# Optimization experiments

Measured on AMD Instinct MI355X. Metric: run time of the kernel, lower is better.

Reference implementation:

```python
import jax, jax.numpy as jnp
import numpy as np

B, S, D_IN, D_VQ, V = 8, 2048, 768, 256, 8192
TEMP = 1.0  # registered buffer, relu(1.0) = 1.0


def setup_inputs() -> dict:
    key = jax.random.key(0)
    k1, k2, k3 = jax.random.split(key, 3)
    x = jax.random.normal(k1, (B, S, D_IN), dtype=jnp.float32)
    W = jax.random.normal(k2, (D_VQ, D_IN), dtype=jnp.float32) * 0.02  # linear weight
    b = jnp.zeros((D_VQ,), dtype=jnp.float32)
    table = jax.random.normal(k3, (V, D_VQ), dtype=jnp.float32)  # learnable_table ~ randn
    return {"x": x, "W": W, "b": b, "table": table}


def reference(x, W, b, table):
    # x: [B,S,D_IN] -> h: [B,S,D_VQ]
    h = jnp.einsum('bsi,di->bsd', x, W) + b
    # negative squared L2 distance to each code: -(|h|^2 + |c|^2 - 2 h.c)
    sim = -(jnp.sum(h * h, axis=-1, keepdims=True)
            + jnp.sum(table * table, axis=-1)
            - 2.0 * jnp.einsum('bsd,vd->bsv', h, table))  # [B,S,V]
    sim = jax.nn.relu(jnp.float32(TEMP)) * sim
    p_code = jax.nn.softmax(sim, axis=-1)
    picked_idx = jnp.argmax(p_code, axis=-1)  # [B,S]
    onehot = jax.nn.one_hot(picked_idx, V, dtype=p_code.dtype)
    # straight-through: hard one-hot forward, soft softmax backward
    p_hard = p_code + jax.lax.stop_gradient(onehot - p_code)
    picked_code = jnp.einsum('bsv,vd->bsd', p_hard, table)  # F.linear(p_hard, table.T)
    # vq_code = x + picked_code - x.detach()  (== picked_code in value)
    vq_code = h + picked_code - jax.lax.stop_gradient(h)
    return vq_code
```

## Files before the change

### kernel.cpp

```cpp
#include <hip/hip_runtime.h>


typedef float f32x4 __attribute__((ext_vector_type(4)));
typedef short s16x8 __attribute__((ext_vector_type(8)));
typedef short s16x4 __attribute__((ext_vector_type(4)));

#define M_TOTAL 16384
#define KDIM 768
#define DQ 256
#define NV 8192
#define MARGIN 1.5f
#define CPB 2048u

#define OFF_TBF   0u
#define OFF_WH    4194304u
#define OFF_WL    4587520u
#define OFF_C2    4980736u
#define OFF_M     5013504u
#define OFF_BEST  5079040u
#define OFF_BCNT  5210112u
#define OFF_CAND  5214208u
#define WS_SINGLE (OFF_CAND + 1024u * CPB * 8u)

static __device__ inline unsigned short bf_rne(float f) {
  unsigned u = __float_as_uint(f);
  u += 0x7FFFu + ((u >> 16) & 1u);
  return (unsigned short)(u >> 16);
}
static __device__ inline unsigned short bf_tr(float f) {
  return (unsigned short)(__float_as_uint(f) >> 16);
}
static __device__ inline float bf_up(unsigned short s) {
  return __uint_as_float(((unsigned)s) << 16);
}
static __device__ inline unsigned mono(float f) {
  unsigned u = __float_as_uint(f);
  return (u & 0x80000000u) ? ~u : (u | 0x80000000u);
}
static __device__ inline float demono(unsigned k) {
  unsigned u = (k & 0x80000000u) ? (k ^ 0x80000000u) : ~k;
  return __uint_as_float(u);
}
static __device__ inline f32x4 mfma16(s16x8 a, s16x8 b, f32x4 c) {
  return __builtin_amdgcn_mfma_f32_16x16x32_bf16(a, b, c, 0, 0, 0);
}

#define PB_TBF 1024
#define PB_C2  32
#define PB_W   192
#define PB_INIT 64

__global__ __launch_bounds__(256) void prep_kernel(
    const float* __restrict__ Wm, const float* __restrict__ table,
    unsigned char* __restrict__ ws) {
  unsigned short* tbf = (unsigned short*)(ws + OFF_TBF);
  unsigned short* Wh  = (unsigned short*)(ws + OFF_WH);
  unsigned short* Wl  = (unsigned short*)(ws + OFF_WL);
  float* c2 = (float*)(ws + OFF_C2);
  unsigned* Mu = (unsigned*)(ws + OFF_M);
  unsigned long long* best = (unsigned long long*)(ws + OFF_BEST);
  const int b = blockIdx.x, t = threadIdx.x;
  if (b < PB_TBF) {
    size_t e0 = ((size_t)b * 256 + t) * 8;
    float4 f0 = *(const float4*)(table + e0);
    float4 f1 = *(const float4*)(table + e0 + 4);
    s16x8 v;
    v[0]=(short)bf_rne(f0.x); v[1]=(short)bf_rne(f0.y);
    v[2]=(short)bf_rne(f0.z); v[3]=(short)bf_rne(f0.w);
    v[4]=(short)bf_rne(f1.x); v[5]=(short)bf_rne(f1.y);
    v[6]=(short)bf_rne(f1.z); v[7]=(short)bf_rne(f1.w);
    *(s16x8*)(tbf + e0) = v;
  } else if (b < PB_TBF + PB_C2) {
    const int v = (b - PB_TBF) * 256 + t;
    const float4* row = (const float4*)(table + (size_t)v * DQ);
    float s = 0.f;
    for (int q = 0; q < 64; ++q) {
      float4 x = row[q];
      s = fmaf(x.x, x.x, s); s = fmaf(x.y, x.y, s);
      s = fmaf(x.z, x.z, s); s = fmaf(x.w, x.w, s);
    }
    c2[v] = s;
  } else if (b < PB_TBF + PB_C2 + PB_W) {
    size_t i = ((size_t)(b - PB_TBF - PB_C2) * 256 + t) * 4;
    float4 f = *(const float4*)(Wm + i);
    float fv[4] = {f.x, f.y, f.z, f.w};
    s16x4 vh, vl;
#pragma unroll
    for (int q = 0; q < 4; ++q) {
      unsigned short hi = bf_tr(fv[q]);
      vh[q] = (short)hi;
      vl[q] = (short)bf_rne(fv[q] - bf_up(hi));
    }
    *(s16x4*)(Wh + i) = vh;
    *(s16x4*)(Wl + i) = vl;
  } else {
    const int i = (b - PB_TBF - PB_C2 - PB_W) * 256 + t;
    Mu[i] = 0u;
    best[i] = 0ull;
  }
}

__global__ __launch_bounds__(256, 3) void h_gemm_kernel(
    const float* __restrict__ x, const float* __restrict__ bias,
    const unsigned char* __restrict__ ws, float* __restrict__ hout) {
  const unsigned short* Whp = (const unsigned short*)(ws + OFF_WH);
  const unsigned short* Wlp = (const unsigned short*)(ws + OFF_WL);
  __shared__ unsigned short xh[128 * 40], xl[128 * 40];
  __shared__ unsigned short wh[64 * 40],  wl[64 * 40];
  const int t = threadIdx.x;
  const int lane = t & 63, wid = t >> 6;
  const int g = lane >> 4, lm = lane & 15;
  const int row_tile = blockIdx.x >> 2, col_tile = blockIdx.x & 3;
  const int r_ld = t >> 1, half = t & 1;
  const int n_ld = t >> 2, qtr = t & 3;

  f32x4 acc[2][4];
#pragma unroll
  for (int i = 0; i < 2; ++i)
#pragma unroll
    for (int j = 0; j < 4; ++j) acc[i][j] = (f32x4)0.f;

  const float* xsrc = x + (size_t)(row_tile * 128 + r_ld) * KDIM + half * 16;
  const unsigned short* whs = Whp + (size_t)(col_tile * 64 + n_ld) * KDIM + qtr * 8;
  const unsigned short* wls = Wlp + (size_t)(col_tile * 64 + n_ld) * KDIM + qtr * 8;

  float4 px[4]; s16x8 pwh, pwl;
#pragma unroll
  for (int q = 0; q < 4; ++q) px[q] = *(const float4*)(xsrc + q * 4);
  pwh = *(const s16x8*)(whs);
  pwl = *(const s16x8*)(wls);

  for (int kc = 0; kc < KDIM / 32; ++kc) {
    __syncthreads();
    {
      float fv[16] = {px[0].x, px[0].y, px[0].z, px[0].w,
                      px[1].x, px[1].y, px[1].z, px[1].w,
                      px[2].x, px[2].y, px[2].z, px[2].w,
                      px[3].x, px[3].y, px[3].z, px[3].w};
      s16x8 vh0, vh1, vl0, vl1;
#pragma unroll
      for (int e = 0; e < 8; ++e) {
        unsigned short hi = bf_tr(fv[e]);
        vh0[e] = (short)hi; vl0[e] = (short)bf_rne(fv[e] - bf_up(hi));
      }
#pragma unroll
      for (int e = 0; e < 8; ++e) {
        unsigned short hi = bf_tr(fv[8 + e]);
        vh1[e] = (short)hi; vl1[e] = (short)bf_rne(fv[8 + e] - bf_up(hi));
      }
      const int xb = r_ld * 40 + half * 16;
      *(s16x8*)&xh[xb] = vh0; *(s16x8*)&xh[xb + 8] = vh1;
      *(s16x8*)&xl[xb] = vl0; *(s16x8*)&xl[xb + 8] = vl1;
      const int wb = n_ld * 40 + qtr * 8;
      *(s16x8*)&wh[wb] = pwh;
      *(s16x8*)&wl[wb] = pwl;
    }
    if (kc + 1 < KDIM / 32) {
      const int k0 = (kc + 1) * 32;
#pragma unroll
      for (int q = 0; q < 4; ++q) px[q] = *(const float4*)(xsrc + k0 + q * 4);
      pwh = *(const s16x8*)(whs + k0);
      pwl = *(const s16x8*)(wls + k0);
    }
    __syncthreads();
    s16x8 ah[2], al[2], bh[4], bl[4];
#pragma unroll
    for (int fr = 0; fr < 2; ++fr) {
      const int rb2 = (wid * 32 + fr * 16 + lm) * 40 + g * 8;
      ah[fr] = *(const s16x8*)&xh[rb2];
      al[fr] = *(const s16x8*)&xl[rb2];
    }
#pragma unroll
    for (int fc = 0; fc < 4; ++fc) {
      const int cb = (fc * 16 + lm) * 40 + g * 8;
      bh[fc] = *(const s16x8*)&wh[cb];
      bl[fc] = *(const s16x8*)&wl[cb];
    }
#pragma unroll
    for (int fr = 0; fr < 2; ++fr)
#pragma unroll
      for (int fc = 0; fc < 4; ++fc) {
        acc[fr][fc] = mfma16(ah[fr], bh[fc], acc[fr][fc]);
        acc[fr][fc] = mfma16(ah[fr], bl[fc], acc[fr][fc]);
        acc[fr][fc] = mfma16(al[fr], bh[fc], acc[fr][fc]);
      }
  }
#pragma unroll
  for (int fc = 0; fc < 4; ++fc) {
    const int col_g = col_tile * 64 + fc * 16 + lm;
    const float bv = bias[col_g];
#pragma unroll
    for (int fr = 0; fr < 2; ++fr) {
      const int row_base = row_tile * 128 + wid * 32 + fr * 16 + g * 4;
#pragma unroll
      for (int r = 0; r < 4; ++r)
        hout[(size_t)(row_base + r) * DQ + col_g] = acc[fr][fc][r] + bv;
    }
  }
}

__global__ __launch_bounds__(256, 3) void scan6_kernel(
    const float* __restrict__ h, const float* __restrict__ table,
    unsigned char* __restrict__ ws) {
  const unsigned short* tbf = (const unsigned short*)(ws + OFF_TBF);
  const float* c2 = (const float*)(ws + OFF_C2);
  unsigned* Mu = (unsigned*)(ws + OFF_M);
  unsigned long long* best = (unsigned long long*)(ws + OFF_BEST);
  unsigned* bcnt = (unsigned*)(ws + OFF_BCNT);
  uint2* cand = (uint2*)(ws + OFF_CAND) + (size_t)blockIdx.x * CPB;
  __shared__ unsigned short bt[2][32 * 256];
  __shared__ unsigned lcnt;

  const int t = threadIdx.x, lane = t & 63, wid = t >> 6;
  const int g4 = lane >> 4, lm = lane & 15;
  const int rb = blockIdx.x >> 3, sp = blockIdx.x & 7;
  const int wrow = rb * 128 + wid * 32;
  const int code0 = sp * 1024;

  if (t == 0) lcnt = 0u;

  s16x8 ah[2][8];
#pragma unroll
  for (int fr = 0; fr < 2; ++fr) {
    const float* hp = h + (size_t)(wrow + fr * 16 + lm) * DQ + g4 * 8;
#pragma unroll
    for (int ks = 0; ks < 8; ++ks) {
      float4 a0 = *(const float4*)(hp + ks * 32);
      float4 a1 = *(const float4*)(hp + ks * 32 + 4);
      s16x8 v;
      v[0]=(short)bf_tr(a0.x); v[1]=(short)bf_tr(a0.y);
      v[2]=(short)bf_tr(a0.z); v[3]=(short)bf_tr(a0.w);
      v[4]=(short)bf_tr(a1.x); v[5]=(short)bf_tr(a1.y);
      v[6]=(short)bf_tr(a1.z); v[7]=(short)bf_tr(a1.w);
      ah[fr][ks] = v;
    }
  }

  float rm[2][4];
#pragma unroll
  for (int fr = 0; fr < 2; ++fr)
#pragma unroll
    for (int r = 0; r < 4; ++r) rm[fr][r] = -3.4e38f;

  int psrc[4], pdst[4];
#pragma unroll
  for (int p = 0; p < 4; ++p) {
    const int o = p * 4096 + t * 16;
    const int code = o >> 9, gsw = (o >> 4) & 31;
    const int gsrc = gsw ^ (code & 7);
    psrc[p] = code * 256 + gsrc * 8;
    pdst[p] = p * 2048 + t * 8;
  }
  const unsigned short* sbase = tbf + (size_t)code0 * DQ;

#define STAGE(buf, tilev)                                                     \
  {                                                                           \
    const unsigned short* s0 = sbase + (size_t)(tilev) * 8192;                \
    _Pragma("unroll")                                                         \
    for (int p = 0; p < 4; ++p)                                               \
      __builtin_amdgcn_global_load_lds(                                       \
          (const unsigned int*)(s0 + psrc[p]),                                \
          (unsigned int*)&bt[buf][pdst[p]], 16, 0, 0);                        \
  }

  STAGE(0, 0);
  __syncthreads();
  int cur = 0;

  for (int tile = 0; tile < 32; ++tile) {
    if (tile + 1 < 32) STAGE(cur ^ 1, tile + 1);

    f32x4 acc[2][2];
#pragma unroll
    for (int fr = 0; fr < 2; ++fr)
#pragma unroll
      for (int fc = 0; fc < 2; ++fc) acc[fr][fc] = (f32x4)0.f;

#pragma unroll
    for (int ks = 0; ks < 8; ++ks) {
      const int gb = ks * 4 + g4;
      const int c0 = lm,      gr0 = gb ^ (c0 & 7);
      const int c1 = 16 + lm, gr1 = gb ^ (c1 & 7);
      s16x8 b0 = *(const s16x8*)&bt[cur][c0 * 256 + gr0 * 8];
      s16x8 b1 = *(const s16x8*)&bt[cur][c1 * 256 + gr1 * 8];
      acc[0][0] = mfma16(ah[0][ks], b0, acc[0][0]);
      acc[1][0] = mfma16(ah[1][ks], b0, acc[1][0]);
      acc[0][1] = mfma16(ah[0][ks], b1, acc[0][1]);
      acc[1][1] = mfma16(ah[1][ks], b1, acc[1][1]);
    }

    float sc[2][2][4];
#pragma unroll
    for (int fc = 0; fc < 2; ++fc) {
      const float cc = c2[code0 + tile * 32 + fc * 16 + lm];
#pragma unroll
      for (int fr = 0; fr < 2; ++fr)
#pragma unroll
        for (int r = 0; r < 4; ++r) {
          const float s = fmaf(2.f, acc[fr][fc][r], -cc);
          sc[fr][fc][r] = s;
          rm[fr][r] = fmaxf(rm[fr][r], s);
        }
    }
#pragma unroll
    for (int fr = 0; fr < 2; ++fr)
#pragma unroll
      for (int r = 0; r < 4; ++r) {
        float v = rm[fr][r];
        v = fmaxf(v, __shfl_xor(v, 1));
        v = fmaxf(v, __shfl_xor(v, 2));
        v = fmaxf(v, __shfl_xor(v, 4));
        v = fmaxf(v, __shfl_xor(v, 8));
        rm[fr][r] = v;
      }

#pragma unroll
    for (int fc = 0; fc < 2; ++fc) {
      const unsigned code_g = (unsigned)(code0 + tile * 32 + fc * 16 + lm);
#pragma unroll
      for (int fr = 0; fr < 2; ++fr)
#pragma unroll
        for (int r = 0; r < 4; ++r) {
          if (sc[fr][fc][r] >= rm[fr][r] - MARGIN) {
            const unsigned row_g = (unsigned)(wrow + fr * 16 + g4 * 4 + r);
            const unsigned idx = atomicAdd(&lcnt, 1u);
            if (idx < CPB) {
              uint2 e;
              e.x = (row_g << 13) | code_g;
              e.y = __float_as_uint(sc[fr][fc][r]);
              cand[idx] = e;
            } else {
              const float4* hp4 = (const float4*)(h + (size_t)row_g * DQ);
              const float4* tp4 = (const float4*)(table + (size_t)code_g * DQ);
              float dot = 0.f;
#pragma unroll 4
              for (int q = 0; q < 64; ++q) {
                float4 a = hp4[q], bb = tp4[q];
                dot = fmaf(a.x, bb.x, dot); dot = fmaf(a.y, bb.y, dot);
                dot = fmaf(a.z, bb.z, dot); dot = fmaf(a.w, bb.w, dot);
              }
              const float sx = fmaf(2.f, dot, -c2[code_g]);
              const unsigned long long key =
                  ((unsigned long long)mono(sx) << 32) |
                  (unsigned long long)(0xFFFFFFFFu - code_g);
              atomicMax(&best[row_g], key);
            }
          }
        }
    }

    __syncthreads();
    cur ^= 1;
  }
#undef STAGE

#pragma unroll
  for (int fr = 0; fr < 2; ++fr)
#pragma unroll
    for (int r = 0; r < 4; ++r)
      if (lm == 0) atomicMax(&Mu[wrow + fr * 16 + g4 * 4 + r], mono(rm[fr][r]));

  __syncthreads();
  if (t == 0) bcnt[blockIdx.x] = (lcnt < CPB) ? lcnt : CPB;
}

__global__ __launch_bounds__(256) void rescore_kernel(
    const float* __restrict__ h, const float* __restrict__ table,
    unsigned char* __restrict__ ws) {
  const float* c2 = (const float*)(ws + OFF_C2);
  const unsigned* Mu = (const unsigned*)(ws + OFF_M);
  unsigned long long* best = (unsigned long long*)(ws + OFF_BEST);
  const unsigned* bcnt = (const unsigned*)(ws + OFF_BCNT);
  const uint2* cand = (const uint2*)(ws + OFF_CAND) + (size_t)blockIdx.x * CPB;

  const unsigned count = bcnt[blockIdx.x];
  const int g = threadIdx.x & 15;
  const unsigned grp = threadIdx.x >> 4;

  for (unsigned i = grp; i < count; i += 16) {
    const uint2 e = cand[i];
    const unsigned row = e.x >> 13, code = e.x & 8191u;
    const float sbf = __uint_as_float(e.y);
    if (sbf < demono(Mu[row]) - MARGIN) continue;
    const float4* hp = (const float4*)(h + (size_t)row * DQ);
    const float4* tp = (const float4*)(table + (size_t)code * DQ);
    float dot = 0.f;
#pragma unroll
    for (int q = 0; q < 4; ++q) {
      float4 a = hp[g * 4 + q], b = tp[g * 4 + q];
      dot = fmaf(a.x, b.x, dot); dot = fmaf(a.y, b.y, dot);
      dot = fmaf(a.z, b.z, dot); dot = fmaf(a.w, b.w, dot);
    }
    dot += __shfl_xor(dot, 1);
    dot += __shfl_xor(dot, 2);
    dot += __shfl_xor(dot, 4);
    dot += __shfl_xor(dot, 8);
    if (g == 0) {
      const float sx = fmaf(2.f, dot, -c2[code]);
      const unsigned long long key =
          ((unsigned long long)mono(sx) << 32) |
          (unsigned long long)(0xFFFFFFFFu - code);
      atomicMax(&best[row], key);
    }
  }
}

template<int MODE>
__global__ __launch_bounds__(256, 3) void scan3_kernel(
    const float* __restrict__ h, const float* __restrict__ table,
    unsigned char* __restrict__ ws) {
  const unsigned short* tbf = (const unsigned short*)(ws + OFF_TBF);
  const float* c2 = (const float*)(ws + OFF_C2);
  unsigned* Mu = (unsigned*)(ws + OFF_M);
  unsigned long long* best = (unsigned long long*)(ws + OFF_BEST);
  __shared__ unsigned short bt[2][32 * 256];

  const int t = threadIdx.x, lane = t & 63, wid = t >> 6;
  const int g4 = lane >> 4, lm = lane & 15;
  const int rb = blockIdx.x >> 3, sp = blockIdx.x & 7;
  const int wrow = rb * 128 + wid * 32;
  const int code0 = sp * 1024;

  s16x8 ah[2][8];
#pragma unroll
  for (int fr = 0; fr < 2; ++fr) {
    const float* hp = h + (size_t)(wrow + fr * 16 + lm) * DQ + g4 * 8;
#pragma unroll
    for (int ks = 0; ks < 8; ++ks) {
      float4 a0 = *(const float4*)(hp + ks * 32);
      float4 a1 = *(const float4*)(hp + ks * 32 + 4);
      s16x8 v;
      v[0]=(short)bf_tr(a0.x); v[1]=(short)bf_tr(a0.y);
      v[2]=(short)bf_tr(a0.z); v[3]=(short)bf_tr(a0.w);
      v[4]=(short)bf_tr(a1.x); v[5]=(short)bf_tr(a1.y);
      v[6]=(short)bf_tr(a1.z); v[7]=(short)bf_tr(a1.w);
      ah[fr][ks] = v;
    }
  }

  float rm[2][4];
#pragma unroll
  for (int fr = 0; fr < 2; ++fr)
#pragma unroll
    for (int r = 0; r < 4; ++r) {
      if (MODE == 2) rm[fr][r] = -3.4e38f;
      else           rm[fr][r] = demono(Mu[wrow + fr * 16 + g4 * 4 + r]);
    }

  int psrc[4], pdst[4];
#pragma unroll
  for (int p = 0; p < 4; ++p) {
    const int o = p * 4096 + t * 16;
    const int code = o >> 9, gsw = (o >> 4) & 31;
    const int gsrc = gsw ^ (code & 7);
    psrc[p] = code * 256 + gsrc * 8;
    pdst[p] = p * 2048 + t * 8;
  }
  const unsigned short* sbase = tbf + (size_t)code0 * DQ;

#define STAGE(buf, tilev)                                                     \
  {                                                                           \
    const unsigned short* s0 = sbase + (size_t)(tilev) * 8192;                \
    _Pragma("unroll")                                                         \
    for (int p = 0; p < 4; ++p)                                               \
      __builtin_amdgcn_global_load_lds(                                       \
          (const unsigned int*)(s0 + psrc[p]),                                \
          (unsigned int*)&bt[buf][pdst[p]], 16, 0, 0);                        \
  }

  STAGE(0, 0);
  __syncthreads();
  int cur = 0;

  for (int tile = 0; tile < 32; ++tile) {
    if (tile + 1 < 32) STAGE(cur ^ 1, tile + 1);

    f32x4 acc[2][2];
#pragma unroll
    for (int fr = 0; fr < 2; ++fr)
#pragma unroll
      for (int fc = 0; fc < 2; ++fc) acc[fr][fc] = (f32x4)0.f;

#pragma unroll
    for (int ks = 0; ks < 8; ++ks) {
      const int gb = ks * 4 + g4;
      const int c0 = lm,      gr0 = gb ^ (c0 & 7);
      const int c1 = 16 + lm, gr1 = gb ^ (c1 & 7);
      s16x8 b0 = *(const s16x8*)&bt[cur][c0 * 256 + gr0 * 8];
      s16x8 b1 = *(const s16x8*)&bt[cur][c1 * 256 + gr1 * 8];
      acc[0][0] = mfma16(ah[0][ks], b0, acc[0][0]);
      acc[1][0] = mfma16(ah[1][ks], b0, acc[1][0]);
      acc[0][1] = mfma16(ah[0][ks], b1, acc[0][1]);
      acc[1][1] = mfma16(ah[1][ks], b1, acc[1][1]);
    }

#pragma unroll
    for (int fc = 0; fc < 2; ++fc) {
      const int code_g = code0 + tile * 32 + fc * 16 + lm;
      const float cc = c2[code_g];
#pragma unroll
      for (int fr = 0; fr < 2; ++fr)
#pragma unroll
        for (int r = 0; r < 4; ++r) {
          const float s = fmaf(2.f, acc[fr][fc][r], -cc);
          if (MODE == 2) {
            rm[fr][r] = fmaxf(rm[fr][r], s);
          } else {
            if (s >= rm[fr][r] - MARGIN) {
              const int row_g = wrow + fr * 16 + g4 * 4 + r;
              const float4* hp4 = (const float4*)(h + (size_t)row_g * DQ);
              const float4* tp4 = (const float4*)(table + (size_t)code_g * DQ);
              float dot = 0.f;
#pragma unroll 4
              for (int q = 0; q < 64; ++q) {
                float4 a = hp4[q], bb = tp4[q];
                dot = fmaf(a.x, bb.x, dot); dot = fmaf(a.y, bb.y, dot);
                dot = fmaf(a.z, bb.z, dot); dot = fmaf(a.w, bb.w, dot);
              }
              const float sx = fmaf(2.f, dot, -cc);
              const unsigned long long key =
                  ((unsigned long long)mono(sx) << 32) |
                  (unsigned long long)(0xFFFFFFFFu - (unsigned)code_g);
              atomicMax(&best[row_g], key);
            }
          }
        }
    }

    __syncthreads();
    cur ^= 1;
  }
#undef STAGE

  if (MODE == 2) {
#pragma unroll
    for (int fr = 0; fr < 2; ++fr)
#pragma unroll
      for (int r = 0; r < 4; ++r) {
        float v = rm[fr][r];
        v = fmaxf(v, __shfl_xor(v, 1));
        v = fmaxf(v, __shfl_xor(v, 2));
        v = fmaxf(v, __shfl_xor(v, 4));
        v = fmaxf(v, __shfl_xor(v, 8));
        if (lm == 0) atomicMax(&Mu[wrow + fr * 16 + g4 * 4 + r], mono(v));
      }
  }
}

__global__ __launch_bounds__(256) void gather_kernel(
    const float* __restrict__ table, const unsigned char* __restrict__ ws,
    float* __restrict__ out) {
  const unsigned long long* best = (const unsigned long long*)(ws + OFF_BEST);
  const int row = blockIdx.x * 64 + (threadIdx.x >> 2);
  const int part = threadIdx.x & 3;
  const unsigned code = 0xFFFFFFFFu - (unsigned)(best[row] & 0xFFFFFFFFull);
  const float4* src = (const float4*)(table + (size_t)code * DQ + part * 64);
  float4* dst = (float4*)(out + (size_t)row * DQ + part * 64);
#pragma unroll
  for (int q = 0; q < 16; ++q) dst[q] = src[q];
}

extern "C" void kernel_launch(void* const* d_in, const int* in_sizes, int n_in,
                              void* d_out, int out_size, void* d_ws, size_t ws_size,
                              hipStream_t stream) {
  const float* x     = (const float*)d_in[0];
  const float* Wm    = (const float*)d_in[1];
  const float* bias  = (const float*)d_in[2];
  const float* table = (const float*)d_in[3];
  float* out = (float*)d_out;
  unsigned char* ws = (unsigned char*)d_ws;

  prep_kernel<<<PB_TBF + PB_C2 + PB_W + PB_INIT, 256, 0, stream>>>(Wm, table, ws);
  h_gemm_kernel<<<512, 256, 0, stream>>>(x, bias, ws, out);

  if (ws_size >= WS_SINGLE) {
    scan6_kernel<<<1024, 256, 0, stream>>>(out, table, ws);
    rescore_kernel<<<1024, 256, 0, stream>>>(out, table, ws);
  } else {
    scan3_kernel<2><<<1024, 256, 0, stream>>>(out, table, ws);
    scan3_kernel<3><<<1024, 256, 0, stream>>>(out, table, ws);
  }

  gather_kernel<<<M_TOTAL / 64, 256, 0, stream>>>(table, ws, out);
}
```

Baseline: 322.8 us.

## Double scan tile rows per wave, use DPP row max, widen gather

```diff
diff --git a/kernel.cpp b/kernel.cpp
--- a/kernel.cpp
+++ b/kernel.cpp
@@ -10,7 +10,8 @@
 #define DQ 256
 #define NV 8192
 #define MARGIN 1.5f
-#define CPB 2048u
+#define CPB 4096u
+#define NSCAN 512u
 
 #define OFF_TBF   0u
 #define OFF_WH    4194304u
@@ -20,7 +21,7 @@
 #define OFF_BEST  5079040u
 #define OFF_BCNT  5210112u
 #define OFF_CAND  5214208u
-#define WS_SINGLE (OFF_CAND + 1024u * CPB * 8u)
+#define WS_SINGLE (OFF_CAND + NSCAN * CPB * 8u)
 
 static __device__ inline unsigned short bf_rne(float f) {
   unsigned u = __float_as_uint(f);
@@ -44,6 +45,12 @@
 static __device__ inline f32x4 mfma16(s16x8 a, s16x8 b, f32x4 c) {
   return __builtin_amdgcn_mfma_f32_16x16x32_bf16(a, b, c, 0, 0, 0);
 }
+#define RORMAX(v, CTRL)                                                       \
+  {                                                                           \
+    int _s = __builtin_amdgcn_update_dpp(0, __float_as_int(v), CTRL, 0xF, 0xF, true); \
+    (v) = fmaxf((v), __int_as_float(_s));                                     \
+  }
+#define RMAX16(v) { RORMAX(v, 0x121) RORMAX(v, 0x122) RORMAX(v, 0x124) RORMAX(v, 0x128) }
 
 #define PB_TBF 1024
 #define PB_C2  32
@@ -199,7 +206,7 @@
   }
 }
 
-__global__ __launch_bounds__(256, 3) void scan6_kernel(
+__global__ __launch_bounds__(256, 2) void scan7_kernel(
     const float* __restrict__ h, const float* __restrict__ table,
     unsigned char* __restrict__ ws) {
   const unsigned short* tbf = (const unsigned short*)(ws + OFF_TBF);
@@ -214,14 +221,14 @@
   const int t = threadIdx.x, lane = t & 63, wid = t >> 6;
   const int g4 = lane >> 4, lm = lane & 15;
   const int rb = blockIdx.x >> 3, sp = blockIdx.x & 7;
-  const int wrow = rb * 128 + wid * 32;
+  const int wrow = rb * 256 + wid * 64;
   const int code0 = sp * 1024;
 
   if (t == 0) lcnt = 0u;
 
-  s16x8 ah[2][8];
-#pragma unroll
-  for (int fr = 0; fr < 2; ++fr) {
+  s16x8 ah[4][8];
+#pragma unroll
+  for (int fr = 0; fr < 4; ++fr) {
     const float* hp = h + (size_t)(wrow + fr * 16 + lm) * DQ + g4 * 8;
 #pragma unroll
     for (int ks = 0; ks < 8; ++ks) {
@@ -236,9 +243,9 @@
     }
   }
 
-  float rm[2][4];
-#pragma unroll
-  for (int fr = 0; fr < 2; ++fr)
+  float rm[4][4];
+#pragma unroll
+  for (int fr = 0; fr < 4; ++fr)
 #pragma unroll
     for (int r = 0; r < 4; ++r) rm[fr][r] = -3.4e38f;
 
@@ -270,9 +277,9 @@
   for (int tile = 0; tile < 32; ++tile) {
     if (tile + 1 < 32) STAGE(cur ^ 1, tile + 1);
 
-    f32x4 acc[2][2];
-#pragma unroll
-    for (int fr = 0; fr < 2; ++fr)
+    f32x4 acc[4][2];
+#pragma unroll
+    for (int fr = 0; fr < 4; ++fr)
 #pragma unroll
       for (int fc = 0; fc < 2; ++fc) acc[fr][fc] = (f32x4)0.f;
 
@@ -283,51 +290,44 @@
       const int c1 = 16 + lm, gr1 = gb ^ (c1 & 7);
       s16x8 b0 = *(const s16x8*)&bt[cur][c0 * 256 + gr0 * 8];
       s16x8 b1 = *(const s16x8*)&bt[cur][c1 * 256 + gr1 * 8];
-      acc[0][0] = mfma16(ah[0][ks], b0, acc[0][0]);
-      acc[1][0] = mfma16(ah[1][ks], b0, acc[1][0]);
-      acc[0][1] = mfma16(ah[0][ks], b1, acc[0][1]);
-      acc[1][1] = mfma16(ah[1][ks], b1, acc[1][1]);
-    }
-
-    float sc[2][2][4];
+#pragma unroll
+      for (int fr = 0; fr < 4; ++fr) {
+        acc[fr][0] = mfma16(ah[fr][ks], b0, acc[fr][0]);
+        acc[fr][1] = mfma16(ah[fr][ks], b1, acc[fr][1]);
+      }
+    }
+
+    const float cc0 = c2[code0 + tile * 32 + lm];
+    const float cc1 = c2[code0 + tile * 32 + 16 + lm];
+#pragma unroll
+    for (int fr = 0; fr < 4; ++fr)
+#pragma unroll
+      for (int r = 0; r < 4; ++r) {
+        float m0 = fmaf(2.f, acc[fr][0][r], -cc0);
+        float m1 = fmaf(2.f, acc[fr][1][r], -cc1);
+        rm[fr][r] = fmaxf(rm[fr][r], fmaxf(m0, m1));
+      }
+#pragma unroll
+    for (int fr = 0; fr < 4; ++fr)
+#pragma unroll
+      for (int r = 0; r < 4; ++r) RMAX16(rm[fr][r])
+
 #pragma unroll
     for (int fc = 0; fc < 2; ++fc) {
-      const float cc = c2[code0 + tile * 32 + fc * 16 + lm];
-#pragma unroll
-      for (int fr = 0; fr < 2; ++fr)
+      const unsigned code_g = (unsigned)(code0 + tile * 32 + fc * 16 + lm);
+      const float cc = fc ? cc1 : cc0;
+#pragma unroll
+      for (int fr = 0; fr < 4; ++fr)
 #pragma unroll
         for (int r = 0; r < 4; ++r) {
           const float s = fmaf(2.f, acc[fr][fc][r], -cc);
-          sc[fr][fc][r] = s;
-          rm[fr][r] = fmaxf(rm[fr][r], s);
-        }
-    }
-#pragma unroll
-    for (int fr = 0; fr < 2; ++fr)
-#pragma unroll
-      for (int r = 0; r < 4; ++r) {
-        float v = rm[fr][r];
-        v = fmaxf(v, __shfl_xor(v, 1));
-        v = fmaxf(v, __shfl_xor(v, 2));
-        v = fmaxf(v, __shfl_xor(v, 4));
-        v = fmaxf(v, __shfl_xor(v, 8));
-        rm[fr][r] = v;
-      }
-
-#pragma unroll
-    for (int fc = 0; fc < 2; ++fc) {
-      const unsigned code_g = (unsigned)(code0 + tile * 32 + fc * 16 + lm);
-#pragma unroll
-      for (int fr = 0; fr < 2; ++fr)
-#pragma unroll
-        for (int r = 0; r < 4; ++r) {
-          if (sc[fr][fc][r] >= rm[fr][r] - MARGIN) {
+          if (s >= rm[fr][r] - MARGIN) {
             const unsigned row_g = (unsigned)(wrow + fr * 16 + g4 * 4 + r);
             const unsigned idx = atomicAdd(&lcnt, 1u);
             if (idx < CPB) {
               uint2 e;
               e.x = (row_g << 13) | code_g;
-              e.y = __float_as_uint(sc[fr][fc][r]);
+              e.y = __float_as_uint(s);
               cand[idx] = e;
             } else {
               const float4* hp4 = (const float4*)(h + (size_t)row_g * DQ);
@@ -355,7 +355,7 @@
 #undef STAGE
 
 #pragma unroll
-  for (int fr = 0; fr < 2; ++fr)
+  for (int fr = 0; fr < 4; ++fr)
 #pragma unroll
     for (int r = 0; r < 4; ++r)
       if (lm == 0) atomicMax(&Mu[wrow + fr * 16 + g4 * 4 + r], mono(rm[fr][r]));
@@ -551,13 +551,13 @@
     const float* __restrict__ table, const unsigned char* __restrict__ ws,
     float* __restrict__ out) {
   const unsigned long long* best = (const unsigned long long*)(ws + OFF_BEST);
-  const int row = blockIdx.x * 64 + (threadIdx.x >> 2);
-  const int part = threadIdx.x & 3;
+  const int row = blockIdx.x * 16 + (threadIdx.x >> 4);
+  const int part = threadIdx.x & 15;
   const unsigned code = 0xFFFFFFFFu - (unsigned)(best[row] & 0xFFFFFFFFull);
-  const float4* src = (const float4*)(table + (size_t)code * DQ + part * 64);
-  float4* dst = (float4*)(out + (size_t)row * DQ + part * 64);
-#pragma unroll
-  for (int q = 0; q < 16; ++q) dst[q] = src[q];
+  const float4* src = (const float4*)(table + (size_t)code * DQ + part * 16);
+  float4* dst = (float4*)(out + (size_t)row * DQ + part * 16);
+#pragma unroll
+  for (int q = 0; q < 4; ++q) dst[q] = src[q];
 }
 
 extern "C" void kernel_launch(void* const* d_in, const int* in_sizes, int n_in,
@@ -574,12 +574,12 @@
   h_gemm_kernel<<<512, 256, 0, stream>>>(x, bias, ws, out);
 
   if (ws_size >= WS_SINGLE) {
-    scan6_kernel<<<1024, 256, 0, stream>>>(out, table, ws);
-    rescore_kernel<<<1024, 256, 0, stream>>>(out, table, ws);
+    scan7_kernel<<<NSCAN, 256, 0, stream>>>(out, table, ws);
+    rescore_kernel<<<NSCAN, 256, 0, stream>>>(out, table, ws);
   } else {
     scan3_kernel<2><<<1024, 256, 0, stream>>>(out, table, ws);
     scan3_kernel<3><<<1024, 256, 0, stream>>>(out, table, ws);
   }
 
-  gather_kernel<<<M_TOTAL / 64, 256, 0, stream>>>(table, ws, out);
-}
+  gather_kernel<<<M_TOTAL / 16, 256, 0, stream>>>(table, ws, out);
+}
```

After: 284.7 us. 11.8% less time.
